# Kernel optimization log

Measured on AMD Instinct MI355X. Metric: run time of the kernel, lower is better.

Reference implementation:

```python
import jax, jax.numpy as jnp
import numpy as np

EPS = 1e-7   # keras backend epsilon used by K.ctc_batch_cost
NEG = -1e30  # log-space -inf surrogate (fp32-safe)


def ctc_batch_cost(labels, y_pred):
    """Faithful jax port of tf.keras.backend.ctc_batch_cost with
    input_length = T and label_length = L for every batch row (as in CTCLayer).
    labels: [B, L] int, values in [0, C-2]; y_pred: [B, T, C] probabilities.
    Blank index = C-1. Returns loss [B, 1]."""
    B, T, C = y_pred.shape
    L = labels.shape[1]
    S = 2 * L + 1
    blank = C - 1
    log_probs = jnp.log(y_pred + EPS)  # [B, T, C]

    # extended label sequence: blank, l1, blank, l2, ..., blank  -> [B, S]
    ext = jnp.full((B, S), blank, dtype=jnp.int32)
    ext = ext.at[:, 1::2].set(labels.astype(jnp.int32))

    # per-frame log-probs of extended labels: [B, T, S]
    lp = jnp.take_along_axis(log_probs, jnp.broadcast_to(ext[:, None, :], (B, T, S)), axis=2)

    # skip transition allowed at s iff ext[s] != blank and ext[s] != ext[s-2]
    skip = jnp.concatenate(
        [jnp.zeros((B, 2), dtype=bool),
         (ext[:, 2:] != ext[:, :-2]) & (ext[:, 2:] != blank)], axis=1)  # [B, S]

    # init alpha at t=0
    alpha0 = jnp.full((B, S), NEG, dtype=log_probs.dtype)
    alpha0 = alpha0.at[:, 0].set(lp[:, 0, 0]).at[:, 1].set(lp[:, 0, 1])

    def step(alpha, lp_t):
        a1 = alpha
        a2 = jnp.pad(alpha[:, :-1], ((0, 0), (1, 0)), constant_values=NEG)
        a3 = jnp.where(skip, jnp.pad(alpha[:, :-2], ((0, 0), (2, 0)), constant_values=NEG), NEG)
        new = jnp.logaddexp(jnp.logaddexp(a1, a2), a3) + lp_t
        return new, None

    # scan over time steps 1..T-1; lp time-major [T-1, B, S]
    alpha, _ = jax.lax.scan(step, alpha0, jnp.swapaxes(lp, 0, 1)[1:])

    loss = -jnp.logaddexp(alpha[:, S - 1], alpha[:, S - 2])  # [B]
    return loss[:, None]  # [B, 1], matching ctc_batch_cost


def setup_inputs() -> dict:
    key = jax.random.key(0)
    k1, k2 = jax.random.split(key)
    y_pred = jax.random.uniform(k1, (256, 512, 512), dtype=jnp.float32)  # probs in (0,1)
    y_true = jax.random.randint(k2, (256, 128), 0, 511)  # labels, blank=511 excluded
    return {"y_true": y_true, "y_pred": y_pred}


def reference(y_true, y_pred):
    return ctc_batch_cost(y_true, y_pred)
```

## Files before the change

### kernel.cpp

```cpp
#include <hip/hip_runtime.h>

namespace {

constexpr int   kT = 512, kC = 512, kL = 128, kBlank = 511;
constexpr int   kCH  = 16;
constexpr int   kNCH = kT / kCH;
constexpr float kEps = 1e-7f, kLn2 = 0.6931471805599453f;

typedef float __attribute__((address_space(1))) f32g;
typedef float __attribute__((address_space(3))) f32l;

__device__ __forceinline__ void glds16(const float* g, float* l) {
    __builtin_amdgcn_global_load_lds((const f32g*)g, (f32l*)l, 16, 0, 0);
}
__device__ __forceinline__ float rlane(float x, int l) {
    return __int_as_float(__builtin_amdgcn_readlane(__float_as_int(x), l));
}
__device__ __forceinline__ float bperm(int a, float x) {
    return __int_as_float(__builtin_amdgcn_ds_bpermute(a, __float_as_int(x)));
}
__device__ __forceinline__ float LOG2(float x) { return __builtin_amdgcn_logf(x); }

__device__ __forceinline__ void barrier_raw() {
    asm volatile("" ::: "memory");
    __builtin_amdgcn_s_barrier();
    asm volatile("" ::: "memory");
}

__global__ __launch_bounds__(128, 1) void ctc_fwd_kernel(
        const int* __restrict__ labels,
        const float* __restrict__ y_pred,
        float* __restrict__ out) {
    __shared__ __align__(16) float buf[2][kCH][kC];

    const int tid  = (int)threadIdx.x;
    const int lane = tid & 63;
    const int wv   = tid >> 6;
    const int b    = (int)blockIdx.x;
    const float* yp  = y_pred + (size_t)b * kT * kC;
    const int*   lab = labels + b * kL;

    int   cls1 = kBlank, cls3 = kBlank;
    float skp1 = 0.f, skp3 = 0.f;
    if (wv == 0) {
        cls1 = lab[2 * lane];
        cls3 = lab[2 * lane + 1];
        skp1 = (lane >= 1 && lab[2 * lane] != lab[2 * lane - 1]) ? 1.f : 0.f;
        skp3 = (lab[2 * lane + 1] != lab[2 * lane]) ? 1.f : 0.f;
    }
    const int addr1 = (lane - 1) << 2;

    float g_rb[kCH], g_r1[kCH], g_r3[kCH];

    if (wv == 1) {
        for (int r = 0; r < kCH; ++r) {
            const float* row = yp + (size_t)r * kC;
            glds16(row + lane * 4,       &buf[0][r][0]);
            glds16(row + 256 + lane * 4, &buf[0][r][256]);
        }
        for (int r = 0; r < kCH; ++r) {
            const float* row = yp + (size_t)(kCH + r) * kC;
            glds16(row + lane * 4,       &buf[1][r][0]);
            glds16(row + 256 + lane * 4, &buf[1][r][256]);
        }
        asm volatile("s_waitcnt vmcnt(32)" ::: "memory");
    }
    barrier_raw();
    if (wv == 0) {
#pragma unroll
        for (int r = 0; r < kCH; ++r) {
            g_rb[r] = buf[0][r][kBlank];
            g_r1[r] = buf[0][r][cls1];
            g_r3[r] = buf[0][r][cls3];
        }
    }
    barrier_raw();

    float a0 = 0.f, a1 = 0.f, a2 = 0.f, a3 = 0.f, a256 = 0.f, etot = 0.f;
    float inj = (lane == 0) ? 1.f : 0.f;

    for (int c = 0; c < kNCH; ++c) {
        if (wv == 1) {
            if (c + 2 < kNCH) {
                float (*bP)[kC] = buf[c & 1];
                for (int r = 0; r < kCH; ++r) {
                    const float* row = yp + (size_t)((c + 2) * kCH + r) * kC;
                    glds16(row + lane * 4,       &bP[r][0]);
                    glds16(row + 256 + lane * 4, &bP[r][256]);
                }
                asm volatile("s_waitcnt vmcnt(32)" ::: "memory");
            } else {
                asm volatile("s_waitcnt vmcnt(0)" ::: "memory");
            }
        } else {
#pragma unroll
            for (int r = 0; r < kCH; ++r) {
                const float pb = g_rb[r] + kEps;
                const float p1 = g_r1[r] + kEps;
                const float p3 = g_r3[r] + kEps;
                float sh3 = bperm(addr1, a3);
                sh3 = (lane == 0) ? 0.f : sh3;
                const float a255 = rlane(a3, 63);
                const float b0 = (a0 + sh3 + inj) * pb;
                const float b1 = (a1 + a0 + skp1 * sh3 + inj) * p1;
                const float b2 = (a2 + a1) * pb;
                const float b3 = (a3 + a2 + skp3 * a1) * p3;
                a256 = (a256 + a255) * pb;
                a0 = b0; a1 = b1; a2 = b2; a3 = b3;
                inj = 0.f;
            }
            if (c & 1) {
                float m = fmaxf(fmaxf(a0, a1), fmaxf(a2, a3));
#pragma unroll
                for (int i = 1; i < 64; i <<= 1) m = fmaxf(m, __shfl_xor(m, i));
                m = fmaxf(m, a256);
                const int ex = (__float_as_int(m) >> 23) & 0xFF;
                if (ex > 1) {
                    const float sc = __int_as_float((254 - ex) << 23);
                    a0 *= sc; a1 *= sc; a2 *= sc; a3 *= sc; a256 *= sc;
                    etot += (float)(ex - 127);
                }
            }
        }
        barrier_raw();
        if (wv == 0 && c + 1 < kNCH) {
            float (*bG)[kC] = buf[(c + 1) & 1];
#pragma unroll
            for (int r = 0; r < kCH; ++r) {
                g_rb[r] = bG[r][kBlank];
                g_r1[r] = bG[r][cls1];
                g_r3[r] = bG[r][cls3];
            }
        }
        barrier_raw();
    }

    if (wv == 0) {
        const float a255 = rlane(a3, 63);
        const float s    = a255 + a256;
        const float loss = -kLn2 * (LOG2(s) + etot);
        if (lane == 0) out[b] = loss;
    }
}

}

extern "C" void kernel_launch(void* const* d_in, const int* in_sizes, int n_in,
                              void* d_out, int out_size, void* d_ws, size_t ws_size,
                              hipStream_t stream) {
    const int*   labels = (const int*)d_in[0];
    const float* y_pred = (const float*)d_in[1];
    float*       out    = (float*)d_out;
    (void)in_sizes; (void)n_in; (void)d_ws; (void)ws_size;
    hipLaunchKernelGGL(ctc_fwd_kernel, dim3(out_size), dim3(128), 0, stream,
                       labels, y_pred, out);
}
```

Before: 52.05 us.

## Triple-buffer LDS chunks and drop the second barrier per chunk

Moves from two LDS buffers to three, rotated by pointer swap, so the loader wave prefetches three chunks ahead. The compute wave now reads the next chunk's gathered probabilities right after its own recurrence, before the one remaining barrier, which removes the second barrier each iteration. The goal is less synchronisation stall on the serial dependency chain. In exchange it uses more shared memory (96KB) and relies on the vmcnt waits being correct for the new three-ahead schedule.

```diff
diff --git a/kernel.cpp b/kernel.cpp
--- a/kernel.cpp
+++ b/kernel.cpp
@@ -31,7 +31,7 @@
         const int* __restrict__ labels,
         const float* __restrict__ y_pred,
         float* __restrict__ out) {
-    __shared__ __align__(16) float buf[2][kCH][kC];
+    __shared__ __align__(16) float buf[3][kCH][kC];
 
     const int tid  = (int)threadIdx.x;
     const int lane = tid & 63;
@@ -52,16 +52,17 @@
 
     float g_rb[kCH], g_r1[kCH], g_r3[kCH];
 
+    float (*bC)[kC] = buf[0];
+    float (*bN)[kC] = buf[1];
+    float (*bP)[kC] = buf[2];
+
     if (wv == 1) {
-        for (int r = 0; r < kCH; ++r) {
-            const float* row = yp + (size_t)r * kC;
-            glds16(row + lane * 4,       &buf[0][r][0]);
-            glds16(row + 256 + lane * 4, &buf[0][r][256]);
-        }
-        for (int r = 0; r < kCH; ++r) {
-            const float* row = yp + (size_t)(kCH + r) * kC;
-            glds16(row + lane * 4,       &buf[1][r][0]);
-            glds16(row + 256 + lane * 4, &buf[1][r][256]);
+        for (int ch = 0; ch < 3; ++ch) {
+            for (int r = 0; r < kCH; ++r) {
+                const float* row = yp + (size_t)(ch * kCH + r) * kC;
+                glds16(row + lane * 4,       &buf[ch][r][0]);
+                glds16(row + 256 + lane * 4, &buf[ch][r][256]);
+            }
         }
         asm volatile("s_waitcnt vmcnt(32)" ::: "memory");
     }
@@ -69,10 +70,11 @@
     if (wv == 0) {
 #pragma unroll
         for (int r = 0; r < kCH; ++r) {
-            g_rb[r] = buf[0][r][kBlank];
-            g_r1[r] = buf[0][r][cls1];
-            g_r3[r] = buf[0][r][cls3];
+            g_rb[r] = bC[r][kBlank];
+            g_r1[r] = bC[r][cls1];
+            g_r3[r] = bC[r][cls3];
         }
+        asm volatile("s_waitcnt lgkmcnt(0)" ::: "memory");
     }
     barrier_raw();
 
@@ -81,15 +83,14 @@
 
     for (int c = 0; c < kNCH; ++c) {
         if (wv == 1) {
-            if (c + 2 < kNCH) {
-                float (*bP)[kC] = buf[c & 1];
+            if (c + 3 < kNCH) {
                 for (int r = 0; r < kCH; ++r) {
-                    const float* row = yp + (size_t)((c + 2) * kCH + r) * kC;
-                    glds16(row + lane * 4,       &bP[r][0]);
-                    glds16(row + 256 + lane * 4, &bP[r][256]);
+                    const float* row = yp + (size_t)((c + 3) * kCH + r) * kC;
+                    glds16(row + lane * 4,       &bC[r][0]);
+                    glds16(row + 256 + lane * 4, &bC[r][256]);
                 }
                 asm volatile("s_waitcnt vmcnt(32)" ::: "memory");
-            } else {
+            } else if (c == kNCH - 3) {
                 asm volatile("s_waitcnt vmcnt(0)" ::: "memory");
             }
         } else {
@@ -121,18 +122,18 @@
                     etot += (float)(ex - 127);
                 }
             }
+            if (c + 1 < kNCH) {
+#pragma unroll
+                for (int r = 0; r < kCH; ++r) {
+                    g_rb[r] = bN[r][kBlank];
+                    g_r1[r] = bN[r][cls1];
+                    g_r3[r] = bN[r][cls3];
+                }
+            }
+            asm volatile("s_waitcnt lgkmcnt(0)" ::: "memory");
         }
         barrier_raw();
-        if (wv == 0 && c + 1 < kNCH) {
-            float (*bG)[kC] = buf[(c + 1) & 1];
-#pragma unroll
-            for (int r = 0; r < kCH; ++r) {
-                g_rb[r] = bG[r][kBlank];
-                g_r1[r] = bG[r][cls1];
-                g_r3[r] = bG[r][cls3];
-            }
-        }
-        barrier_raw();
+        float (*tmp)[kC] = bC; bC = bN; bN = bP; bP = tmp;
     }
 
     if (wv == 0) {
```

New measurement: 54.28 us. 1.04x slower.
